# Optimization experiments

Hardware: AMD Instinct MI355X
Metric: run time of the kernel (lower is better)

Reference implementation:

```python
import jax, jax.numpy as jnp
import numpy as np

M_NODES = 49152  # HEALPix nside=64


def setup_inputs() -> dict:
    key = jax.random.key(0)
    ks = jax.random.split(key, 7)
    N, M, Fin, Fout, K, dm = 16, M_NODES, 32, 64, 5, 1
    E = 8 * M
    x = jax.random.normal(ks[0], (N, M, Fin), dtype=jnp.float32)
    # sparse Laplacian in COO form; small values keep Chebyshev recursion stable
    edge_vals = jax.random.normal(ks[1], (E,), dtype=jnp.float32) * 0.2
    edge_rows = jax.random.randint(ks[2], (E,), 0, M, dtype=jnp.int32)
    edge_cols = jax.random.randint(ks[3], (E,), 0, M, dtype=jnp.int32)
    dkernel = jax.random.normal(ks[4], (Fin, dm, K), dtype=jnp.float32) * (2.0 / K) ** 0.5
    pkernel = jax.random.normal(ks[5], (Fout, Fin * dm), dtype=jnp.float32) * (2.0 / (Fin * dm)) ** 0.5
    bias = jax.random.normal(ks[6], (1, 1, Fout), dtype=jnp.float32) * 0.01
    return {"x": x, "edge_vals": edge_vals, "dkernel": dkernel,
            "pkernel": pkernel, "bias": bias,
            "edge_rows": edge_rows, "edge_cols": edge_cols}


def reference(x, edge_vals, dkernel, pkernel, bias, edge_rows, edge_cols):
    N, M, Fin = x.shape
    _, dm, K = dkernel.shape
    Fout = pkernel.shape[0]

    def spmm(v):  # L @ v with L in COO, v: [M, C]
        return jax.ops.segment_sum(edge_vals[:, None] * v[edge_cols], edge_rows,
                                   num_segments=M)

    # x0: [M, N*Fin]
    x0 = jnp.transpose(x, (1, 0, 2)).reshape(M, N * Fin)
    stack = [x0]
    if K > 1:
        x1 = spmm(x0)
        stack.append(x1)
    for k in range(2, K):  # Chebyshev recursion T_k = 2 L T_{k-1} - T_{k-2}
        x2 = 2.0 * spmm(x1) - x0
        stack.append(x2)
        x0, x1 = x1, x2
    xs = jnp.stack(stack, axis=0)                      # [K, M, N*Fin]
    xs = xs.reshape(K, M, N, Fin)
    xs = jnp.transpose(xs, (3, 0, 2, 1)).reshape(Fin, K, N * M)
    y = jnp.einsum('fdk,fkp->fdp', dkernel, xs)        # depthwise: [Fin, dm, N*M]
    y = y.reshape(Fin * dm, N * M)
    y = pkernel @ y                                    # pointwise: [Fout, N*M]
    y = y.T.reshape(N, M, Fout)
    y = y + bias
    return jax.nn.relu(y)
```

## Files before the change

### kernel.cpp

```cpp
#include <hip/hip_runtime.h>


#define M_NODES 49152
#define FIN 32
#define KCH 5
#define FOUT 64
#define NB 16

typedef unsigned int u32;
typedef unsigned short u16;
typedef short bf16x8 __attribute__((ext_vector_type(8)));
typedef float f32x4 __attribute__((ext_vector_type(4)));

__device__ __forceinline__ float bflo(u32 w) { union { float f; u32 i; } v; v.i = w << 16; return v.f; }
__device__ __forceinline__ float bfhi(u32 w) { union { float f; u32 i; } v; v.i = w & 0xffff0000u; return v.f; }
__device__ __forceinline__ u32 f2bf(float f) {
    union { float f; u32 i; } v; v.f = f;
    u32 r = v.i + 0x7fffu + ((v.i >> 16) & 1u);
    return r >> 16;
}
__device__ __forceinline__ u32 pack2(float a, float b) { return f2bf(a) | (f2bf(b) << 16); }

__global__ void count_kernel(const int* __restrict__ rows, int* __restrict__ cnt, int E) {
    int e = blockIdx.x * 256 + threadIdx.x;
    if (e < E) atomicAdd(&cnt[rows[e]], 1);
}

__global__ __launch_bounds__(1024) void scan_kernel(int* __restrict__ cf,
                                                    int* __restrict__ row_ptr, int M) {
    const int CH = M_NODES / 1024;
    int tid = threadIdx.x;
    int lane = tid & 63;
    int wid = tid >> 6;
    int base = tid * CH;

    int4 v[CH / 4];
    const int4* src = (const int4*)(cf + base);
    int sum = 0;
    #pragma unroll
    for (int j = 0; j < CH / 4; ++j) {
        v[j] = src[j];
        sum += v[j].x + v[j].y + v[j].z + v[j].w;
    }
    int x = sum;
    #pragma unroll
    for (int off = 1; off < 64; off <<= 1) {
        int y = __shfl_up(x, off, 64);
        if (lane >= off) x += y;
    }
    __shared__ int wsum[16];
    if (lane == 63) wsum[wid] = x;
    __syncthreads();
    if (tid < 16) {
        int w = wsum[tid];
        int xx = w;
        #pragma unroll
        for (int off = 1; off < 16; off <<= 1) {
            int y = __shfl_up(xx, off, 64);
            if (tid >= off) xx += y;
        }
        wsum[tid] = xx - w;
    }
    __syncthreads();
    int run = (x - sum) + wsum[wid];
    int4* rp = (int4*)(row_ptr + base);
    int4* cc = (int4*)(cf + base);
    #pragma unroll
    for (int j = 0; j < CH / 4; ++j) {
        int4 o;
        o.x = run;           run += v[j].x;
        o.y = run;           run += v[j].y;
        o.z = run;           run += v[j].z;
        o.w = run;           run += v[j].w;
        rp[j] = o;
        cc[j] = o;
    }
    if (tid == 1023) row_ptr[M] = run;
}

__global__ void scatter_kernel(const int* __restrict__ rows, const int* __restrict__ cols,
                               const float* __restrict__ vals, int* __restrict__ fill,
                               int2* __restrict__ edges, int E) {
    int e = blockIdx.x * 256 + threadIdx.x;
    if (e < E) {
        int r = rows[e];
        int pos = atomicAdd(&fill[r], 1);
        int2 ed; ed.x = cols[e]; ed.y = __float_as_int(vals[e]);
        edges[pos] = ed;
    }
}

__global__ __launch_bounds__(256) void cast_transpose_kernel(
    const float* __restrict__ x, uint4* __restrict__ T0, int M) {
    int m = blockIdx.x * 4 + (threadIdx.x >> 6);
    int l = threadIdx.x & 63;
    int n = l >> 2;
    int f0 = (l & 3) * 8;
    const float4* xp = (const float4*)(x + ((size_t)n * M + m) * FIN + f0);
    float4 a = xp[0], b = xp[1];
    uint4 o;
    o.x = pack2(a.x, a.y); o.y = pack2(a.z, a.w);
    o.z = pack2(b.x, b.y); o.w = pack2(b.z, b.w);
    T0[(size_t)m * 64 + l] = o;
}

__global__ void wprep_kernel(const float* __restrict__ dk, const float* __restrict__ pk,
                             u16* __restrict__ W) {
    int t = blockIdx.x * 256 + threadIdx.x;
    if (t < FOUT * KCH * FIN) {
        int fo = t / (KCH * FIN);
        int kf = t % (KCH * FIN);
        int kc = kf / FIN;
        int f  = kf % FIN;
        W[fo * (KCH * FIN) + kf] = (u16)f2bf(pk[fo * FIN + f] * dk[f * KCH + kc]);
    }
}

__device__ __forceinline__ void acc8(float* r, uint4 g, float v) {
    r[0] = fmaf(v, bflo(g.x), r[0]); r[1] = fmaf(v, bfhi(g.x), r[1]);
    r[2] = fmaf(v, bflo(g.y), r[2]); r[3] = fmaf(v, bfhi(g.y), r[3]);
    r[4] = fmaf(v, bflo(g.z), r[4]); r[5] = fmaf(v, bfhi(g.z), r[5]);
    r[6] = fmaf(v, bflo(g.w), r[6]); r[7] = fmaf(v, bfhi(g.w), r[7]);
}

template<int FIRST>
__global__ __launch_bounds__(256) void spmm_kernel(
    const uint4* __restrict__ Tin, const uint4* __restrict__ Tprev, uint4* __restrict__ Tout,
    const int* __restrict__ row_ptr, const int2* __restrict__ edges, int M) {
    int m = blockIdx.x * 4 + (threadIdx.x >> 6);
    int l = threadIdx.x & 63;
    int e = row_ptr[m];
    int e_end = row_ptr[m + 1];
    uint4 p;
    if (!FIRST) p = Tprev[(size_t)m * 64 + l];
    float r[8] = {0.f, 0.f, 0.f, 0.f, 0.f, 0.f, 0.f, 0.f};
    for (; e + 8 <= e_end; e += 8) {
        int2 ed[8];
        #pragma unroll
        for (int j = 0; j < 8; ++j) ed[j] = edges[e + j];
        uint4 g[8];
        #pragma unroll
        for (int j = 0; j < 8; ++j) g[j] = Tin[(size_t)ed[j].x * 64 + l];
        #pragma unroll
        for (int j = 0; j < 8; ++j) acc8(r, g[j], __int_as_float(ed[j].y));
    }
    if (e + 4 <= e_end) {
        int2 ed[4];
        #pragma unroll
        for (int j = 0; j < 4; ++j) ed[j] = edges[e + j];
        uint4 g[4];
        #pragma unroll
        for (int j = 0; j < 4; ++j) g[j] = Tin[(size_t)ed[j].x * 64 + l];
        #pragma unroll
        for (int j = 0; j < 4; ++j) acc8(r, g[j], __int_as_float(ed[j].y));
        e += 4;
    }
    for (; e < e_end; ++e) {
        int2 ed = edges[e];
        uint4 g = Tin[(size_t)ed.x * 64 + l];
        acc8(r, g, __int_as_float(ed.y));
    }
    if (!FIRST) {
        r[0] = fmaf(2.f, r[0], -bflo(p.x)); r[1] = fmaf(2.f, r[1], -bfhi(p.x));
        r[2] = fmaf(2.f, r[2], -bflo(p.y)); r[3] = fmaf(2.f, r[3], -bfhi(p.y));
        r[4] = fmaf(2.f, r[4], -bflo(p.z)); r[5] = fmaf(2.f, r[5], -bfhi(p.z));
        r[6] = fmaf(2.f, r[6], -bflo(p.w)); r[7] = fmaf(2.f, r[7], -bfhi(p.w));
    }
    uint4 o;
    o.x = pack2(r[0], r[1]); o.y = pack2(r[2], r[3]);
    o.z = pack2(r[4], r[5]); o.w = pack2(r[6], r[7]);
    Tout[(size_t)m * 64 + l] = o;
}

__global__ __launch_bounds__(256) void pw_mfma_kernel(
    const uint4* __restrict__ T, const uint4* __restrict__ W4,
    const float* __restrict__ bias, float* __restrict__ out, int M) {
    __shared__ uint4 lds[2][1024];
    int t = threadIdx.x;
    int w = t >> 6;
    int l = t & 63;
    int lr = l & 15;
    int lg = l >> 4;
    int m0 = blockIdx.x * 16;
    const size_t kstride = (size_t)M * 64;
    const uint4* tile_base = T + (size_t)m0 * 64;

    float bv[4];
    #pragma unroll
    for (int fo = 0; fo < 4; ++fo) bv[fo] = bias[fo * 16 + lr];

    f32x4 acc[4][4];
    #pragma unroll
    for (int nn = 0; nn < 4; ++nn)
        #pragma unroll
        for (int fo = 0; fo < 4; ++fo)
            acc[nn][fo] = (f32x4){bv[fo], bv[fo], bv[fo], bv[fo]};

    uint4 sreg[4];
    #pragma unroll
    for (int j = 0; j < 4; ++j) sreg[j] = tile_base[(size_t)j * 256 + t];
    #pragma unroll
    for (int j = 0; j < 4; ++j) {
        int idx = j * 256 + t;
        int row = idx >> 6, c = idx & 63;
        lds[0][row * 64 + (c ^ (row & 7))] = sreg[j];
    }
    __syncthreads();

    for (int kc = 0; kc < KCH; ++kc) {
        uint4 nreg[4];
        if (kc < KCH - 1) {
            const uint4* src = tile_base + (size_t)(kc + 1) * kstride;
            #pragma unroll
            for (int j = 0; j < 4; ++j) nreg[j] = src[(size_t)j * 256 + t];
        }
        bf16x8 bfr[4];
        #pragma unroll
        for (int fo = 0; fo < 4; ++fo) {
            uint4 wv = W4[(fo * 16 + lr) * 20 + kc * 4 + lg];
            bfr[fo] = *(bf16x8*)&wv;
        }
        const uint4* buf = lds[kc & 1];
        #pragma unroll
        for (int nn = 0; nn < 4; ++nn) {
            int n_g = w * 4 + nn;
            uint4 a = buf[lr * 64 + ((n_g * 4 + lg) ^ (lr & 7))];
            bf16x8 af = *(bf16x8*)&a;
            #pragma unroll
            for (int fo = 0; fo < 4; ++fo)
                acc[nn][fo] = __builtin_amdgcn_mfma_f32_16x16x32_bf16(af, bfr[fo], acc[nn][fo], 0, 0, 0);
        }
        if (kc < KCH - 1) {
            uint4* buf2 = lds[(kc + 1) & 1];
            #pragma unroll
            for (int j = 0; j < 4; ++j) {
                int idx = j * 256 + t;
                int row = idx >> 6, c = idx & 63;
                buf2[row * 64 + (c ^ (row & 7))] = nreg[j];
            }
        }
        __syncthreads();
    }

    #pragma unroll
    for (int nn = 0; nn < 4; ++nn) {
        int n_g = w * 4 + nn;
        #pragma unroll
        for (int fo = 0; fo < 4; ++fo) {
            float* op = out + ((size_t)n_g * M + m0 + lg * 4) * FOUT + fo * 16 + lr;
            #pragma unroll
            for (int rr = 0; rr < 4; ++rr)
                __builtin_nontemporal_store(fmaxf(acc[nn][fo][rr], 0.f), op + (size_t)rr * FOUT);
        }
    }
}

extern "C" void kernel_launch(void* const* d_in, const int* in_sizes, int n_in,
                              void* d_out, int out_size, void* d_ws, size_t ws_size,
                              hipStream_t stream) {
    const float* x         = (const float*)d_in[0];
    const float* edge_vals = (const float*)d_in[1];
    const float* dk        = (const float*)d_in[2];
    const float* pk        = (const float*)d_in[3];
    const float* bias      = (const float*)d_in[4];
    const int*   erow      = (const int*)d_in[5];
    const int*   ecol      = (const int*)d_in[6];
    float* out = (float*)d_out;

    const int M = M_NODES;
    const int E = in_sizes[1];

    size_t t_words = (size_t)M * 64;
    uint4* T       = (uint4*)d_ws;
    u16*   W       = (u16*)(T + 5 * t_words);
    int*   row_ptr = (int*)(W + FOUT * KCH * FIN);
    int*   fill    = row_ptr + (M + 4);
    int2*  edges   = (int2*)(fill + M);

    uint4* T0 = T;
    uint4* T1 = T + 1 * t_words;
    uint4* T2 = T + 2 * t_words;
    uint4* T3 = T + 3 * t_words;
    uint4* T4 = T + 4 * t_words;

    hipMemsetAsync(fill, 0, (size_t)M * sizeof(int), stream);
    count_kernel<<<(E + 255) / 256, 256, 0, stream>>>(erow, fill, E);
    scan_kernel<<<1, 1024, 0, stream>>>(fill, row_ptr, M);
    scatter_kernel<<<(E + 255) / 256, 256, 0, stream>>>(erow, ecol, edge_vals, fill, edges, E);

    cast_transpose_kernel<<<M / 4, 256, 0, stream>>>(x, T0, M);
    wprep_kernel<<<(FOUT * KCH * FIN + 255) / 256, 256, 0, stream>>>(dk, pk, W);

    spmm_kernel<1><<<M / 4, 256, 0, stream>>>(T0, T0, T1, row_ptr, edges, M);
    spmm_kernel<0><<<M / 4, 256, 0, stream>>>(T1, T0, T2, row_ptr, edges, M);
    spmm_kernel<0><<<M / 4, 256, 0, stream>>>(T2, T1, T3, row_ptr, edges, M);
    spmm_kernel<0><<<M / 4, 256, 0, stream>>>(T3, T2, T4, row_ptr, edges, M);

    pw_mfma_kernel<<<M / 16, 256, 0, stream>>>(T, (const uint4*)W, bias, out, M);
}
```

Baseline: 440.9 us.

## Stage all Chebyshev tiles via direct-to-LDS loads, coalesce output, vectorize CSR build

The pointwise MFMA kernel now stages all five Chebyshev tiles into LDS up front using global_load_lds, replacing the register double-buffered loop. It also routes results through LDS so each lane writes 16-byte output vectors. Separately, the count and scatter kernels read four edges per thread with vector loads, and the cast-transpose kernel uses nontemporal loads. The larger LDS footprint (80KB per block) may reduce occupancy, and the vectorized edge kernels assume E is divisible by 4.

```diff
diff --git a/kernel.cpp b/kernel.cpp
--- a/kernel.cpp
+++ b/kernel.cpp
@@ -21,9 +21,21 @@
 }
 __device__ __forceinline__ u32 pack2(float a, float b) { return f2bf(a) | (f2bf(b) << 16); }
 
-__global__ void count_kernel(const int* __restrict__ rows, int* __restrict__ cnt, int E) {
+__device__ __forceinline__ void stage_row(const uint4* gsrc, uint4* ldst) {
+    __builtin_amdgcn_global_load_lds(
+        (const __attribute__((address_space(1))) unsigned int*)gsrc,
+        (__attribute__((address_space(3))) unsigned int*)ldst, 16, 0, 0);
+}
+
+__global__ void count_kernel(const int* __restrict__ rows, int* __restrict__ cnt, int E4) {
     int e = blockIdx.x * 256 + threadIdx.x;
-    if (e < E) atomicAdd(&cnt[rows[e]], 1);
+    if (e < E4) {
+        int4 r = ((const int4*)rows)[e];
+        atomicAdd(&cnt[r.x], 1);
+        atomicAdd(&cnt[r.y], 1);
+        atomicAdd(&cnt[r.z], 1);
+        atomicAdd(&cnt[r.w], 1);
+    }
 }
 
 __global__ __launch_bounds__(1024) void scan_kernel(int* __restrict__ cf,
@@ -80,13 +92,17 @@
 
 __global__ void scatter_kernel(const int* __restrict__ rows, const int* __restrict__ cols,
                                const float* __restrict__ vals, int* __restrict__ fill,
-                               int2* __restrict__ edges, int E) {
+                               int2* __restrict__ edges, int E4) {
     int e = blockIdx.x * 256 + threadIdx.x;
-    if (e < E) {
-        int r = rows[e];
-        int pos = atomicAdd(&fill[r], 1);
-        int2 ed; ed.x = cols[e]; ed.y = __float_as_int(vals[e]);
-        edges[pos] = ed;
+    if (e < E4) {
+        int4 r = ((const int4*)rows)[e];
+        int4 c = ((const int4*)cols)[e];
+        float4 v = ((const float4*)vals)[e];
+        int pos;
+        pos = atomicAdd(&fill[r.x], 1); edges[pos] = (int2){c.x, __float_as_int(v.x)};
+        pos = atomicAdd(&fill[r.y], 1); edges[pos] = (int2){c.y, __float_as_int(v.y)};
+        pos = atomicAdd(&fill[r.z], 1); edges[pos] = (int2){c.z, __float_as_int(v.z)};
+        pos = atomicAdd(&fill[r.w], 1); edges[pos] = (int2){c.w, __float_as_int(v.w)};
     }
 }
 
@@ -96,11 +112,12 @@
     int l = threadIdx.x & 63;
     int n = l >> 2;
     int f0 = (l & 3) * 8;
-    const float4* xp = (const float4*)(x + ((size_t)n * M + m) * FIN + f0);
-    float4 a = xp[0], b = xp[1];
+    const f32x4* xp = (const f32x4*)(x + ((size_t)n * M + m) * FIN + f0);
+    f32x4 a = __builtin_nontemporal_load(xp);
+    f32x4 b = __builtin_nontemporal_load(xp + 1);
     uint4 o;
-    o.x = pack2(a.x, a.y); o.y = pack2(a.z, a.w);
-    o.z = pack2(b.x, b.y); o.w = pack2(b.z, b.w);
+    o.x = pack2(a[0], a[1]); o.y = pack2(a[2], a[3]);
+    o.z = pack2(b[0], b[1]); o.w = pack2(b[2], b[3]);
     T0[(size_t)m * 64 + l] = o;
 }
 
@@ -175,7 +192,7 @@
 __global__ __launch_bounds__(256) void pw_mfma_kernel(
     const uint4* __restrict__ T, const uint4* __restrict__ W4,
     const float* __restrict__ bias, float* __restrict__ out, int M) {
-    __shared__ uint4 lds[2][1024];
+    __shared__ uint4 lds4[5 * 1024];
     int t = threadIdx.x;
     int w = t >> 6;
     int l = t & 63;
@@ -183,74 +200,67 @@
     int lg = l >> 4;
     int m0 = blockIdx.x * 16;
     const size_t kstride = (size_t)M * 64;
-    const uint4* tile_base = T + (size_t)m0 * 64;
-
-    float bv[4];
-    #pragma unroll
-    for (int fo = 0; fo < 4; ++fo) bv[fo] = bias[fo * 16 + lr];
-
-    f32x4 acc[4][4];
-    #pragma unroll
-    for (int nn = 0; nn < 4; ++nn)
-        #pragma unroll
-        for (int fo = 0; fo < 4; ++fo)
-            acc[nn][fo] = (f32x4){bv[fo], bv[fo], bv[fo], bv[fo]};
-
-    uint4 sreg[4];
-    #pragma unroll
-    for (int j = 0; j < 4; ++j) sreg[j] = tile_base[(size_t)j * 256 + t];
-    #pragma unroll
-    for (int j = 0; j < 4; ++j) {
-        int idx = j * 256 + t;
-        int row = idx >> 6, c = idx & 63;
-        lds[0][row * 64 + (c ^ (row & 7))] = sreg[j];
-    }
-    __syncthreads();
-
-    for (int kc = 0; kc < KCH; ++kc) {
-        uint4 nreg[4];
-        if (kc < KCH - 1) {
-            const uint4* src = tile_base + (size_t)(kc + 1) * kstride;
-            #pragma unroll
-            for (int j = 0; j < 4; ++j) nreg[j] = src[(size_t)j * 256 + t];
-        }
-        bf16x8 bfr[4];
+
+    bf16x8 bfr[KCH][4];
+    #pragma unroll
+    for (int kc = 0; kc < KCH; ++kc)
         #pragma unroll
         for (int fo = 0; fo < 4; ++fo) {
             uint4 wv = W4[(fo * 16 + lr) * 20 + kc * 4 + lg];
-            bfr[fo] = *(bf16x8*)&wv;
-        }
-        const uint4* buf = lds[kc & 1];
+            bfr[kc][fo] = *(bf16x8*)&wv;
+        }
+    f32x4 acc[4][4];
+    #pragma unroll
+    for (int fo = 0; fo < 4; ++fo) {
+        float bv = bias[fo * 16 + lr];
+        #pragma unroll
+        for (int nn = 0; nn < 4; ++nn)
+            acc[nn][fo] = (f32x4){bv, bv, bv, bv};
+    }
+
+    #pragma unroll
+    for (int kc = 0; kc < KCH; ++kc) {
+        #pragma unroll
+        for (int i = 0; i < 4; ++i) {
+            int row = w * 4 + i;
+            const uint4* gsrc = T + (size_t)kc * kstride + (size_t)(m0 + row) * 64
+                                  + (l ^ (row & 7));
+            stage_row(gsrc, &lds4[kc * 1024 + row * 64]);
+        }
+    }
+    __syncthreads();
+
+    #pragma unroll
+    for (int kc = 0; kc < KCH; ++kc) {
         #pragma unroll
         for (int nn = 0; nn < 4; ++nn) {
-            int n_g = w * 4 + nn;
-            uint4 a = buf[lr * 64 + ((n_g * 4 + lg) ^ (lr & 7))];
+            int n = w * 4 + nn;
+            uint4 a = lds4[kc * 1024 + lr * 64 + ((n * 4 + lg) ^ (lr & 7))];
             bf16x8 af = *(bf16x8*)&a;
             #pragma unroll
             for (int fo = 0; fo < 4; ++fo)
-                acc[nn][fo] = __builtin_amdgcn_mfma_f32_16x16x32_bf16(af, bfr[fo], acc[nn][fo], 0, 0, 0);
-        }
-        if (kc < KCH - 1) {
-            uint4* buf2 = lds[(kc + 1) & 1];
-            #pragma unroll
-            for (int j = 0; j < 4; ++j) {
-                int idx = j * 256 + t;
-                int row = idx >> 6, c = idx & 63;
-                buf2[row * 64 + (c ^ (row & 7))] = nreg[j];
-            }
-        }
-        __syncthreads();
-    }
-
+                acc[nn][fo] = __builtin_amdgcn_mfma_f32_16x16x32_bf16(af, bfr[kc][fo], acc[nn][fo], 0, 0, 0);
+        }
+    }
+    __syncthreads();
+
+    float* zone = (float*)lds4 + w * 1088;
     #pragma unroll
     for (int nn = 0; nn < 4; ++nn) {
-        int n_g = w * 4 + nn;
-        #pragma unroll
-        for (int fo = 0; fo < 4; ++fo) {
-            float* op = out + ((size_t)n_g * M + m0 + lg * 4) * FOUT + fo * 16 + lr;
+        int n = w * 4 + nn;
+        #pragma unroll
+        for (int fo = 0; fo < 4; ++fo)
             #pragma unroll
             for (int rr = 0; rr < 4; ++rr)
-                __builtin_nontemporal_store(fmaxf(acc[nn][fo][rr], 0.f), op + (size_t)rr * FOUT);
+                zone[(lg * 4 + rr) * 68 + fo * 16 + lr] = acc[nn][fo][rr];
+        #pragma unroll
+        for (int i = 0; i < 4; ++i) {
+            int mrow = i * 4 + lg;
+            f32x4 v = *(const f32x4*)&zone[mrow * 68 + lr * 4];
+            v[0] = fmaxf(v[0], 0.f); v[1] = fmaxf(v[1], 0.f);
+            v[2] = fmaxf(v[2], 0.f); v[3] = fmaxf(v[3], 0.f);
+            f32x4* op = (f32x4*)(out + ((size_t)n * M + m0 + mrow) * FOUT + lr * 4);
+            __builtin_nontemporal_store(v, op);
         }
     }
 }
@@ -284,9 +294,9 @@
     uint4* T4 = T + 4 * t_words;
 
     hipMemsetAsync(fill, 0, (size_t)M * sizeof(int), stream);
-    count_kernel<<<(E + 255) / 256, 256, 0, stream>>>(erow, fill, E);
+    count_kernel<<<(E / 4 + 255) / 256, 256, 0, stream>>>(erow, fill, E / 4);
     scan_kernel<<<1, 1024, 0, stream>>>(fill, row_ptr, M);
-    scatter_kernel<<<(E + 255) / 256, 256, 0, stream>>>(erow, ecol, edge_vals, fill, edges, E);
+    scatter_kernel<<<(E / 4 + 255) / 256, 256, 0, stream>>>(erow, ecol, edge_vals, fill, edges, E / 4);
 
     cast_transpose_kernel<<<M / 4, 256, 0, stream>>>(x, T0, M);
     wprep_kernel<<<(FOUT * KCH * FIN + 255) / 256, 256, 0, stream>>>(dk, pk, W);
```

Result: faster. 425.4 us (-3.5%).
